# Kernel tuning notes

Hardware: AMD Instinct MI355X
Metric: run time of the kernel (lower is better)

The kernel has to match this reference:

```python
import jax, jax.numpy as jnp
import numpy as np
from jax import lax

B, T, D, H, W = 2, 8, 64, 64, 64
E, HID = 4, 256


def _layernorm(x, g, b, eps=1e-5):
    m = x.mean(-1, keepdims=True)
    v = ((x - m) ** 2).mean(-1, keepdims=True)
    return (x - m) / jnp.sqrt(v + eps) * g + b


def _pscan(A, X, axis):
    # linear recurrence h_t = A_t * h_{t-1} + X_t via associative scan
    def comb(l, r):
        a1, x1 = l
        a2, x2 = r
        return a2 * a1, a2 * x1 + x2
    return lax.associative_scan(comb, (A, X), axis=axis)[1]


def setup_inputs() -> dict:
    key = jax.random.key(0)
    ks = jax.random.split(key, 32)
    r = lambda i, shape, s=1.0: jax.random.normal(ks[i], shape, jnp.float32) * s
    D2 = 2 * D
    return {
        'x_re': r(0, (B, T, D, H, W)), 'x_im': r(1, (B, T, D, H, W)),
        'dt': jax.random.uniform(ks[2], (T,), jnp.float32, 0.5, 1.0),
        'ln_s_g': jnp.ones(D2), 'ln_s_b': jnp.zeros(D2),
        'conv_w': r(3, (3, 3, D2, D2), 0.03), 'conv_b': jnp.zeros(D2),
        'mom_w': r(4, (D2, D2), 0.08), 'mom_b': jnp.zeros(D2),
        'adv_w': jnp.full((1,), 0.1, jnp.float32),
        'enc_re': r(5, (D, D), 0.1), 'enc_im': r(6, (D, D), 0.1),
        'dec_re': r(7, (D, D), 0.1), 'dec_im': r(8, (D, D), 0.1),
        'flux_a_re': r(9, (D,)), 'flux_a_im': r(10, (D,), 0.1),
        'fin_re': r(11, (D, D), 0.1), 'fin_im': r(12, (D, D), 0.1),
        'fproj_re': r(13, (D, D), 0.1), 'fproj_im': r(14, (D, D), 0.1),
        'gate_w': r(15, (D2, D), 0.1), 'gate_b': jnp.zeros(D),
        'lam_re': r(16, (D,)), 'lam_im': r(17, (D,), 0.1),
        'noise_re': r(18, (B, T, H, W, D)), 'noise_im': r(19, (B, T, H, W, D)),
        'e_scale': jnp.full((1,), 0.1, jnp.float32),
        'ln_t_g': jnp.ones(D2), 'ln_t_b': jnp.zeros(D2),
        'router_w': r(20, (D2, E), 0.1), 'router_b': jnp.zeros(E),
        'w1': r(21, (E, D2, HID), 0.08), 'b1': jnp.zeros((E, HID)),
        'w2': r(22, (E, HID, D2), 0.08), 'b2': jnp.zeros((E, D2)),
    }


def _forward(x_re, x_im, dt, ln_s_g, ln_s_b, conv_w, conv_b, mom_w, mom_b, adv_w,
             enc_re, enc_im, dec_re, dec_im, flux_a_re, flux_a_im, fin_re, fin_im,
             fproj_re, fproj_im, gate_w, gate_b, lam_re, lam_im, noise_re, noise_im,
             e_scale, ln_t_g, ln_t_b, router_w, router_b, w1, b1, w2, b2):
    x = (x_re + 1j * x_im).astype(jnp.complex64)            # [B,T,D,H,W]
    target_energy = (jnp.abs(x) ** 2).mean(axis=(-2, -1))   # [B,T,D]
    momentum = x.mean(axis=(-2, -1))                        # [B,T,D] complex
    xcl = jnp.transpose(x, (0, 1, 3, 4, 2))                 # [B,T,H,W,D]
    Bs, Ts, Hs, Ws, Ds = xcl.shape
    D2 = 2 * Ds
    # --- spatial complex (Clifford) conv branch: LN over 2D channels + conv ---
    xr = jnp.concatenate([xcl.real, xcl.imag], -1)          # [B,T,H,W,2D]
    xn = _layernorm(xr, ln_s_g, ln_s_b)
    y = lax.conv_general_dilated(xn.reshape(Bs * Ts, Hs, Ws, D2), conv_w,
                                 (1, 1), 'SAME',
                                 dimension_numbers=('NHWC', 'HWIO', 'NHWC')) + conv_b
    y = y.reshape(Bs, Ts, Hs, Ws, D2)
    xcl = xcl + (y[..., :Ds] + 1j * y[..., Ds:])
    # --- momentum advection ---
    z_mean = xcl.mean(axis=(2, 3))                          # [B,T,D]
    mom_cat = jnp.concatenate([momentum.real, momentum.imag], -1) @ mom_w + mom_b
    mom_new = mom_cat[..., :Ds] + 1j * mom_cat[..., Ds:]
    dtb = jnp.broadcast_to(dt[None, :], (Bs, Ts))
    xcl = xcl + (mom_new * adv_w[0])[:, :, None, None, :] * dtb[:, :, None, None, None]
    momentum = 0.9 * momentum + 0.1 * z_mean
    # --- eigenbasis encode ---
    x_eigen = xcl @ (enc_re + 1j * enc_im)                  # [B,T,H,W,D]
    x_mean = x_eigen.mean(axis=(2, 3))                      # [B,T,D]
    # --- flux tracker: parallel scan over T ---
    A_flux = jnp.exp(-jax.nn.softplus(flux_a_re) + 1j * flux_a_im)
    A_flux = jnp.broadcast_to(A_flux, (Bs, Ts, Ds)).astype(jnp.complex64)
    X_flux = x_mean @ (fin_re + 1j * fin_im)
    flux_seq = _pscan(A_flux, X_flux, axis=1)               # [B,T,D]
    source = flux_seq @ (fproj_re + 1j * fproj_im)
    gate = jax.nn.sigmoid(jnp.concatenate([flux_seq.real, flux_seq.imag], -1) @ gate_w + gate_b)
    g = gate[:, :, None, None, :]
    forcing = x_eigen * g + source[:, :, None, None, :] * (1.0 - g)
    # --- temporal propagation: per-site parallel scan over T ---
    lam = -jax.nn.softplus(lam_re) + 1j * lam_im            # [D]
    op_decay = jnp.exp(lam[None, None, :] * dtb[:, :, None])  # [B,T,D]
    op_forcing = (op_decay - 1.0) / lam
    u_t = forcing * op_forcing[:, :, None, None, :]
    A_time = jnp.broadcast_to(op_decay[:, :, None, None, :], u_t.shape)
    u_out = _pscan(A_time, u_t, axis=1)                     # [B,T,H,W,D]
    noise = 0.01 * jnp.sqrt(dtb)[:, :, None, None, None] * (noise_re + 1j * noise_im)
    u_out = u_out + noise
    # --- decode + energy projection ---
    x_out = u_out @ (dec_re + 1j * dec_im)                  # [B,T,H,W,D]
    cur_e = (jnp.abs(x_out) ** 2).mean(axis=(2, 3))
    ratio = jnp.clip(target_energy / (cur_e + 1e-8), 0.5, 2.0)
    sf = jnp.sqrt(ratio)[:, :, None, None, :]
    x_out = x_out * (1.0 + e_scale[0] * (sf - 1.0))
    # --- temporal LN + MoE FFN on real-concat tokens ---
    xr2 = jnp.concatenate([x_out.real, x_out.imag], -1)
    xn2 = _layernorm(xr2, ln_t_g, ln_t_b)                   # [B,T,H,W,2D]
    tok = xn2.reshape(-1, D2)                               # [N,2D]
    p = jax.nn.softmax(tok @ router_w + router_b, -1)       # [N,E]
    hmid = jax.nn.gelu(jnp.einsum('nd,edh->neh', tok, w1) + b1)
    eout = jnp.einsum('neh,ehd->ned', hmid, w2) + b2
    out_tok = tok + jnp.einsum('ne,ned->nd', p, eout)
    out = out_tok.reshape(Bs, Ts, Hs, Ws, D2)
    x_out_c = out[..., :Ds] + 1j * out[..., Ds:]
    z_out = xcl + x_out_c
    z = jnp.transpose(z_out, (0, 1, 4, 2, 3))               # [B,T,D,H,W]
    return jnp.stack([z.real, z.imag])                      # [2,B,T,D,H,W]


def reference(x_re, x_im, dt, ln_s_g, ln_s_b, conv_w, conv_b, mom_w, mom_b, adv_w,
              enc_re, enc_im, dec_re, dec_im, flux_a_re, flux_a_im, fin_re, fin_im,
              fproj_re, fproj_im, gate_w, gate_b, lam_re, lam_im, noise_re, noise_im,
              e_scale, ln_t_g, ln_t_b, router_w, router_b, w1, b1, w2, b2):
    return _forward(x_re, x_im, dt, ln_s_g, ln_s_b, conv_w, conv_b, mom_w, mom_b, adv_w,
                    enc_re, enc_im, dec_re, dec_im, flux_a_re, flux_a_im, fin_re, fin_im,
                    fproj_re, fproj_im, gate_w, gate_b, lam_re, lam_im, noise_re, noise_im,
                    e_scale, ln_t_g, ln_t_b, router_w, router_b, w1, b1, w2, b2)
```

## Files before the change

### kernel.cpp

```cpp
#include <hip/hip_runtime.h>
#include <hip/hip_bf16.h>
#include <math.h>


#define W_XB     4194304u
#define W_C      8388608u
#define W_CWT    12582912u
#define W_W1T    14680064u
#define W_W2T    14745600u
#define W_ENCM   14811136u
#define W_DECM   14819328u
#define W_XMP_RE 14827520u
#define W_XMP_IM 14893056u
#define W_EP_RE  14958592u
#define W_EP_IM  15220736u
#define W_XMR    15482880u
#define W_XMI    15483904u
#define W_FLR    15484928u
#define W_FLI    15485952u
#define W_EIG_RE 16777216u
#define W_K1R    20971520u
#define W_K1I    21037056u
#define W_K1E    21102592u
#define W_SMALL  25165824u
#define W_TE     (W_SMALL+0u)
#define W_MTRE   (W_SMALL+3072u)
#define W_MTIM   (W_SMALL+4096u)
#define W_GATE   (W_SMALL+5120u)
#define W_SRCRE  (W_SMALL+6144u)
#define W_SRCIM  (W_SMALL+7168u)
#define W_OPFRE  (W_SMALL+8192u)
#define W_OPFIM  (W_SMALL+9216u)
#define W_OPDRE  (W_SMALL+10240u)
#define W_OPDIM  (W_SMALL+11264u)
#define W_SCALE  (W_SMALL+12288u)

#define XB_IM 4194304u

typedef __attribute__((ext_vector_type(8))) short bf16x8;
typedef __attribute__((ext_vector_type(4))) float f32x4;

__device__ __forceinline__ unsigned short bfr(float x) {
  __hip_bfloat16 h = __float2bfloat16(x);
  return *(unsigned short*)&h;
}
__device__ __forceinline__ unsigned int pk2(float a, float b) {
  return ((unsigned int)bfr(b) << 16) | (unsigned int)bfr(a);
}
__device__ __forceinline__ float sb2f(short s) {
  return __uint_as_float(((unsigned int)(unsigned short)s) << 16);
}
__device__ __forceinline__ float softplusf(float x) {
  return (x > 20.f) ? x : log1pf(expf(x));
}

__global__ __launch_bounds__(256) void k2_transpose_ln(
    const float* __restrict__ xre, const float* __restrict__ xim,
    const float* __restrict__ g, const float* __restrict__ bb_, float* ws) {
  int blk = blockIdx.x; int bt = blk >> 6, h = blk & 63;
  __shared__ float tre[64][65], tim[64][65];
  __shared__ float mean_l[64], rstd_l[64];
  int tid = threadIdx.x;
  size_t inbase = (size_t)bt * 262144 + (size_t)h * 64;
  for (int i = tid; i < 1024; i += 256) {
    int d = i >> 4, w4 = (i & 15) * 4;
    float4 vr = *(const float4*)&xre[inbase + (size_t)d * 4096 + w4];
    float4 vi = *(const float4*)&xim[inbase + (size_t)d * 4096 + w4];
    tre[d][w4] = vr.x; tre[d][w4 + 1] = vr.y; tre[d][w4 + 2] = vr.z; tre[d][w4 + 3] = vr.w;
    tim[d][w4] = vi.x; tim[d][w4 + 1] = vi.y; tim[d][w4 + 2] = vi.z; tim[d][w4 + 3] = vi.w;
  }
  __syncthreads();
  {
    int w = tid >> 2, part = tid & 3;
    float s = 0.f, sq = 0.f;
    for (int dd = part * 16; dd < part * 16 + 16; dd++) {
      float vr = tre[dd][w], vi = tim[dd][w];
      s += vr + vi; sq += vr * vr + vi * vi;
    }
    s += __shfl_xor(s, 1);  s += __shfl_xor(s, 2);
    sq += __shfl_xor(sq, 1); sq += __shfl_xor(sq, 2);
    if (part == 0) {
      float m = s / 128.f, v = sq / 128.f - m * m;
      mean_l[w] = m; rstd_l[w] = rsqrtf(v + 1e-5f);
    }
  }
  {
    int d = tid >> 2, part = tid & 3;
    float sr = 0.f, si = 0.f, se = 0.f;
    for (int w2 = part * 16; w2 < part * 16 + 16; w2++) {
      float vr = tre[d][w2], vi = tim[d][w2];
      sr += vr; si += vi; se += vr * vr + vi * vi;
    }
    sr += __shfl_xor(sr, 1); sr += __shfl_xor(sr, 2);
    si += __shfl_xor(si, 1); si += __shfl_xor(si, 2);
    se += __shfl_xor(se, 1); se += __shfl_xor(se, 2);
    if (part == 0) {
      int idx = h * 1024 + bt * 64 + d;
      ws[W_K1R + idx] = sr; ws[W_K1I + idx] = si; ws[W_K1E + idx] = se;
    }
  }
  {
    __hip_bfloat16* xbb = (__hip_bfloat16*)(ws + W_XB);
    for (int i = tid; i < 1024; i += 256) {
      int d = i >> 4, w4 = (i & 15) * 4;
      size_t ob = (size_t)(bt * 64 + d) * 4096 + (size_t)h * 64 + w4;
      *(unsigned int*)&xbb[ob]     = pk2(tre[d][w4],     tre[d][w4 + 1]);
      *(unsigned int*)&xbb[ob + 2] = pk2(tre[d][w4 + 2], tre[d][w4 + 3]);
      *(unsigned int*)&xbb[XB_IM + ob]     = pk2(tim[d][w4],     tim[d][w4 + 1]);
      *(unsigned int*)&xbb[XB_IM + ob + 2] = pk2(tim[d][w4 + 2], tim[d][w4 + 3]);
    }
  }
  __syncthreads();
  size_t tokbase = (size_t)blk * 64;
  __hip_bfloat16* xnb = (__hip_bfloat16*)(ws + W_C);
  int c0 = (tid & 63) * 2, wg = tid >> 6;
  float gc0 = g[c0], bc0 = bb_[c0], gc1 = g[c0 + 1], bc1 = bb_[c0 + 1];
  for (int pass = 0; pass < 16; pass++) {
    int w = pass * 4 + wg;
    float m = mean_l[w], rs = rstd_l[w];
    float v0 = (c0 < 64) ? tre[c0][w] : tim[c0 - 64][w];
    float v1 = (c0 + 1 < 64) ? tre[c0 + 1][w] : tim[c0 + 1 - 64][w];
    *(unsigned int*)&xnb[tokbase * 128 + (size_t)w * 128 + c0] =
        pk2((v0 - m) * rs * gc0 + bc0, (v1 - m) * rs * gc1 + bc1);
  }
}

__global__ void k1b2b(const float* __restrict__ mom_w, const float* __restrict__ mom_b,
                      const float* __restrict__ adv_w, const float* __restrict__ dt, float* ws) {
  int bt = blockIdx.x; int t = bt & 7;
  __shared__ float mc[128], outl[128];
  int tid = threadIdx.x;
  if (tid < 64) {
    int d = tid;
    float a = 0.f, b = 0.f, c = 0.f;
    for (int h = 0; h < 64; h++) {
      int idx = h * 1024 + bt * 64 + d;
      a += ws[W_K1R + idx]; b += ws[W_K1I + idx]; c += ws[W_K1E + idx];
    }
    ws[W_TE + bt * 64 + d] = c / 4096.f;
    mc[d] = a / 4096.f;
    mc[64 + d] = b / 4096.f;
  }
  __syncthreads();
  float acc = mom_b[tid];
  for (int k = 0; k < 128; k++) acc += mc[k] * mom_w[k * 128 + tid];
  outl[tid] = acc;
  __syncthreads();
  if (tid < 64) {
    float f = adv_w[0] * dt[t];
    ws[W_MTRE + bt * 64 + tid] = outl[tid] * f;
    ws[W_MTIM + bt * 64 + tid] = outl[64 + tid] * f;
  }
}

__global__ void k0_wprep(const float* __restrict__ w1, const float* __restrict__ w2,
                         const float* __restrict__ cw,
                         const float* __restrict__ enc_re, const float* __restrict__ enc_im,
                         const float* __restrict__ dec_re, const float* __restrict__ dec_im,
                         float* ws) {
  __hip_bfloat16* w1f = (__hip_bfloat16*)(ws + W_W1T);
  __hip_bfloat16* w2f = (__hip_bfloat16*)(ws + W_W2T);
  __hip_bfloat16* cwt = (__hip_bfloat16*)(ws + W_CWT);
  __hip_bfloat16* encM = (__hip_bfloat16*)(ws + W_ENCM);
  __hip_bfloat16* decM = (__hip_bfloat16*)(ws + W_DECM);
  int idx = blockIdx.x * 256 + threadIdx.x;
  if (idx < 131072) {
    {
      int j = idx & 7, lane = (idx >> 3) & 63, kt = (idx >> 9) & 3, nt = (idx >> 11) & 15, e = idx >> 15;
      int cout = nt * 16 + (lane & 15);
      int cin = kt * 32 + (lane >> 4) * 8 + j;
      w1f[idx] = __float2bfloat16(w1[((size_t)(e * 128 + cin)) * 256 + cout]);
    }
    {
      int j = idx & 7, lane = (idx >> 3) & 63, kt = (idx >> 9) & 7, nt = (idx >> 12) & 7, e = idx >> 15;
      int cout = nt * 16 + (lane & 15);
      int cin = kt * 32 + (lane >> 4) * 8 + j;
      w2f[idx] = __float2bfloat16(w2[((size_t)(e * 256 + cin)) * 128 + cout]);
    }
  }
  if (idx < 147456) {
    int j = idx & 7, lane = (idx >> 3) & 63, kt = (idx >> 9) & 3, r = idx >> 11;
    int nt = r & 7, tap = r >> 3;
    int cout = nt * 16 + (lane & 15);
    int cin = kt * 32 + (lane >> 4) * 8 + j;
    cwt[idx] = __float2bfloat16(cw[((size_t)(tap * 128 + cin)) * 128 + cout]);
  }
  if (idx < 16384) {
    int jj = idx & 7, lane = (idx >> 3) & 63, kt = (idx >> 9) & 3, nt = idx >> 11;
    int jc = nt * 16 + (lane & 15);
    int k = kt * 32 + (lane >> 4) * 8 + jj;
    float ve, vd;
    if (k < 64) {
      ve = (jc < 64) ? enc_re[k * 64 + jc] : enc_im[k * 64 + (jc - 64)];
      vd = (jc < 64) ? dec_re[k * 64 + jc] : dec_im[k * 64 + (jc - 64)];
    } else {
      int kk = k - 64;
      ve = (jc < 64) ? -enc_im[kk * 64 + jc] : enc_re[kk * 64 + (jc - 64)];
      vd = (jc < 64) ? -dec_im[kk * 64 + jc] : dec_re[kk * 64 + (jc - 64)];
    }
    encM[idx] = __float2bfloat16(ve);
    decM[idx] = __float2bfloat16(vd);
  }
}

__global__ __launch_bounds__(256) void k3_conv_enc(const float* __restrict__ cb, float* ws) {
  int blk = blockIdx.x; int bt = blk >> 6, h = blk & 63;
  const __hip_bfloat16* xnb = (const __hip_bfloat16*)(ws + W_C);
  const __hip_bfloat16* cwt = (const __hip_bfloat16*)(ws + W_CWT);
  const __hip_bfloat16* encM = (const __hip_bfloat16*)(ws + W_ENCM);
  const __hip_bfloat16* xbb = (const __hip_bfloat16*)(ws + W_XB);
  __hip_bfloat16* xclb = (__hip_bfloat16*)ws;
  __hip_bfloat16* eigb = (__hip_bfloat16*)(ws + W_EIG_RE);
  __shared__ __align__(16) char smem[3 * 66 * 136 * 2];
  __hip_bfloat16 (*xin)[66][136] = (__hip_bfloat16(*)[66][136])smem;
  char* A = smem;
  int tid = threadIdx.x, lane = tid & 63, wv = tid >> 6;
  int arow = lane & 15, kgrp = (lane >> 4) * 8, rbase = (lane >> 4) * 4;

  for (int r = 0; r < 3; r++) {
    int hh = h + r - 1;
    if (hh < 0 || hh >= 64) {
      unsigned int* z = (unsigned int*)&xin[r][0][0];
      for (int i = tid; i < 4488; i += 256) z[i] = 0u;
    } else {
      if (tid < 68) *(unsigned int*)&xin[r][0][tid * 2] = 0u;
      else if (tid < 136) *(unsigned int*)&xin[r][65][(tid - 136 + 68) * 2] = 0u;
      const __hip_bfloat16* src = xnb + ((size_t)bt * 4096 + (size_t)hh * 64) * 128;
      for (int i = tid; i < 1024; i += 256) {
        int wp = (i >> 4) + 1, c8 = (i & 15) * 8;
        *(bf16x8*)&xin[r][wp][c8] = *(const bf16x8*)&src[(size_t)(wp - 1) * 128 + c8];
      }
    }
  }
  __syncthreads();

  f32x4 oacc[4][2];
  #pragma unroll
  for (int m = 0; m < 4; m++) {
    oacc[m][0] = (f32x4){0.f, 0.f, 0.f, 0.f};
    oacc[m][1] = (f32x4){0.f, 0.f, 0.f, 0.f};
  }

  for (int tap = 0; tap < 9; tap++) {
    int kh = tap / 3, kw = tap % 3;
    const __hip_bfloat16* wt0 = cwt + ((size_t)(tap * 8 + wv * 2) * 4) * 512 + lane * 8;
    #pragma unroll
    for (int kt = 0; kt < 4; kt++) {
      bf16x8 a[4];
      #pragma unroll
      for (int m = 0; m < 4; m++)
        a[m] = *(const bf16x8*)&xin[kh][m * 16 + arow + kw][kt * 32 + kgrp];
      bf16x8 b0 = *(const bf16x8*)&wt0[(size_t)kt * 512];
      bf16x8 b1 = *(const bf16x8*)&wt0[(size_t)(kt + 4) * 512];
      #pragma unroll
      for (int m = 0; m < 4; m++) {
        oacc[m][0] = __builtin_amdgcn_mfma_f32_16x16x32_bf16(a[m], b0, oacc[m][0], 0, 0, 0);
        oacc[m][1] = __builtin_amdgcn_mfma_f32_16x16x32_bf16(a[m], b1, oacc[m][1], 0, 0, 0);
      }
    }
  }
  __syncthreads();

  size_t rowtok = (size_t)blk * 64;
  #pragma unroll
  for (int n = 0; n < 2; n++) {
    int cout = (wv * 2 + n) * 16 + arow;
    bool isre = cout < 64;
    int d = cout & 63;
    float add = cb[cout] + ws[(isre ? W_MTRE : W_MTIM) + bt * 64 + d];
    size_t xb = isre ? 0u : XB_IM;
    const __hip_bfloat16* xsrc = xbb + xb + (size_t)(bt * 64 + d) * 4096 + (size_t)h * 64;
    #pragma unroll
    for (int m = 0; m < 4; m++) {
      unsigned int u0 = *(const unsigned int*)&xsrc[m * 16 + rbase];
      unsigned int u1 = *(const unsigned int*)&xsrc[m * 16 + rbase + 2];
      float xo0 = __uint_as_float(u0 << 16);
      float xo1 = __uint_as_float(u0 & 0xffff0000u);
      float xo2 = __uint_as_float(u1 << 16);
      float xo3 = __uint_as_float(u1 & 0xffff0000u);
      #pragma unroll
      for (int r = 0; r < 4; r++) {
        int w = m * 16 + rbase + r;
        float xo = (r == 0) ? xo0 : (r == 1) ? xo1 : (r == 2) ? xo2 : xo3;
        float v = xo + oacc[m][n][r] + add;
        xclb[xb + (rowtok + w) * 64 + d] = __float2bfloat16(v);
        *(__hip_bfloat16*)(A + w * 256 + ((cout * 2) ^ ((w & 7) << 4))) = __float2bfloat16(v);
      }
    }
  }
  __syncthreads();

  f32x4 acc[4][2];
  #pragma unroll
  for (int m = 0; m < 4; m++) {
    acc[m][0] = (f32x4){0.f, 0.f, 0.f, 0.f};
    acc[m][1] = (f32x4){0.f, 0.f, 0.f, 0.f};
  }
  #pragma unroll
  for (int kt = 0; kt < 4; kt++) {
    bf16x8 a[4];
    #pragma unroll
    for (int m = 0; m < 4; m++)
      a[m] = *(const bf16x8*)(A + (m * 16 + arow) * 256 + (((kt * 32 + kgrp) * 2) ^ ((arow & 7) << 4)));
    bf16x8 b0 = *(const bf16x8*)&encM[(((size_t)(wv * 2 + 0) * 4 + kt) * 64 + lane) * 8];
    bf16x8 b1 = *(const bf16x8*)&encM[(((size_t)(wv * 2 + 1) * 4 + kt) * 64 + lane) * 8];
    #pragma unroll
    for (int m = 0; m < 4; m++) {
      acc[m][0] = __builtin_amdgcn_mfma_f32_16x16x32_bf16(a[m], b0, acc[m][0], 0, 0, 0);
      acc[m][1] = __builtin_amdgcn_mfma_f32_16x16x32_bf16(a[m], b1, acc[m][1], 0, 0, 0);
    }
  }
  #pragma unroll
  for (int n = 0; n < 2; n++) {
    int jc = (wv * 2 + n) * 16 + arow;
    size_t eb = (jc < 64) ? 0u : XB_IM;
    int col = jc & 63;
    #pragma unroll
    for (int m = 0; m < 4; m++)
      #pragma unroll
      for (int r = 0; r < 4; r++)
        eigb[eb + (rowtok + m * 16 + rbase + r) * 64 + col] = __float2bfloat16(acc[m][n][r]);
    float s = 0.f;
    #pragma unroll
    for (int m = 0; m < 4; m++)
      #pragma unroll
      for (int r = 0; r < 4; r++) s += acc[m][n][r];
    s += __shfl_xor(s, 16);
    s += __shfl_xor(s, 32);
    if (lane < 16)
      ws[(jc < 64 ? W_XMP_RE : W_XMP_IM) + (size_t)blk * 64 + col] = s;
  }
}

__global__ void k6a_xm(float* ws) {
  int bt = blockIdx.x, j = threadIdx.x;
  float sr = 0.f, si = 0.f;
  for (int q = 0; q < 64; q++) {
    sr += ws[W_XMP_RE + (size_t)(bt * 64 + q) * 64 + j];
    si += ws[W_XMP_IM + (size_t)(bt * 64 + q) * 64 + j];
  }
  ws[W_XMR + bt * 64 + j] = sr / 4096.f;
  ws[W_XMI + bt * 64 + j] = si / 4096.f;
}

__global__ void k6b_flux(const float* __restrict__ fin_re, const float* __restrict__ fin_im,
                         const float* __restrict__ flux_a_re, const float* __restrict__ flux_a_im,
                         float* ws) {
  __shared__ float Xfr[1024], Xfi[1024];
  int tid = threadIdx.x;
  for (int i = tid; i < 1024; i += 256) {
    int bt = i >> 6, j = i & 63;
    float ar = 0.f, ai = 0.f;
    for (int d = 0; d < 64; d++) {
      float xr = ws[W_XMR + bt * 64 + d], xi = ws[W_XMI + bt * 64 + d];
      float wr = fin_re[d * 64 + j], wi = fin_im[d * 64 + j];
      ar += xr * wr - xi * wi; ai += xr * wi + xi * wr;
    }
    Xfr[i] = ar; Xfi[i] = ai;
  }
  __syncthreads();
  if (tid < 128) {
    int b = tid >> 6, j = tid & 63;
    float mag = expf(-softplusf(flux_a_re[j]));
    float aar = mag * cosf(flux_a_im[j]), aai = mag * sinf(flux_a_im[j]);
    float sr = 0.f, si = 0.f;
    for (int t = 0; t < 8; t++) {
      int idx = (b * 8 + t) * 64 + j;
      float nr = aar * sr - aai * si + Xfr[idx];
      float ni = aar * si + aai * sr + Xfi[idx];
      sr = nr; si = ni;
      ws[W_FLR + idx] = sr; ws[W_FLI + idx] = si;
    }
  }
}

__global__ void k6c_gate(const float* __restrict__ fproj_re, const float* __restrict__ fproj_im,
                         const float* __restrict__ gate_w, const float* __restrict__ gate_b,
                         const float* __restrict__ lam_re, const float* __restrict__ lam_im,
                         const float* __restrict__ dt, float* ws) {
  int bt = blockIdx.x;
  __shared__ float flr[64], fli[64];
  int tid = threadIdx.x;
  if (tid < 64) { flr[tid] = ws[W_FLR + bt * 64 + tid]; fli[tid] = ws[W_FLI + bt * 64 + tid]; }
  __syncthreads();
  int j = tid >> 2, part = tid & 3;
  float ar = 0.f, ai = 0.f, lg = 0.f;
  for (int d = part * 16; d < part * 16 + 16; d++) {
    float fr = flr[d], fi = fli[d];
    float wr = fproj_re[d * 64 + j], wi = fproj_im[d * 64 + j];
    ar += fr * wr - fi * wi; ai += fr * wi + fi * wr;
    lg += fr * gate_w[d * 64 + j] + fi * gate_w[(64 + d) * 64 + j];
  }
  ar += __shfl_xor(ar, 1); ar += __shfl_xor(ar, 2);
  ai += __shfl_xor(ai, 1); ai += __shfl_xor(ai, 2);
  lg += __shfl_xor(lg, 1); lg += __shfl_xor(lg, 2);
  if (part == 0) {
    int idx = bt * 64 + j;
    ws[W_SRCRE + idx] = ar; ws[W_SRCIM + idx] = ai;
    ws[W_GATE + idx] = 1.f / (1.f + expf(-(lg + gate_b[j])));
  }
  if (tid < 64) {
    int d = tid, t = bt & 7;
    float lr = -softplusf(lam_re[d]), li = lam_im[d];
    float dtv = dt[t];
    float mag = expf(lr * dtv);
    float dr = mag * cosf(li * dtv), di = mag * sinf(li * dtv);
    int idx = bt * 64 + d;
    ws[W_OPDRE + idx] = dr; ws[W_OPDIM + idx] = di;
    float omr = dr - 1.f, omi = di;
    float den = lr * lr + li * li;
    ws[W_OPFRE + idx] = (omr * lr + omi * li) / den;
    ws[W_OPFIM + idx] = (omi * lr - omr * li) / den;
  }
}

__global__ __launch_bounds__(256) void k7_dec(const float* __restrict__ nre,
                                              const float* __restrict__ nim,
                                              const float* __restrict__ dt, float* ws) {
  int blk = blockIdx.x;
  int b = blk >> 8, h = (blk >> 2) & 63, wq = blk & 3;
  const __hip_bfloat16* decM = (const __hip_bfloat16*)(ws + W_DECM);
  __hip_bfloat16* eigb = (__hip_bfloat16*)(ws + W_EIG_RE);
  __shared__ float gl[8][64], srl[8][64], sil[8][64], ofr[8][64], ofi[8][64], odr[8][64], odi[8][64];
  __shared__ __align__(16) char A[2][4096];
  __shared__ float dts[8];
  int tid = threadIdx.x, lane = tid & 63, wv = tid >> 6;
  int arow = lane & 15, kgrp = (lane >> 4) * 8, rbase = (lane >> 4) * 4;
  for (int i = tid; i < 512; i += 256) {
    int t = i >> 6, d = i & 63, idx = (b * 8 + t) * 64 + d;
    gl[t][d]  = ws[W_GATE + idx];
    srl[t][d] = ws[W_SRCRE + idx]; sil[t][d] = ws[W_SRCIM + idx];
    ofr[t][d] = ws[W_OPFRE + idx]; ofi[t][d] = ws[W_OPFIM + idx];
    odr[t][d] = ws[W_OPDRE + idx]; odi[t][d] = ws[W_OPDIM + idx];
  }
  if (tid < 8) dts[tid] = dt[tid];
  __syncthreads();

  int dp = (tid & 31) * 2, wslot = tid >> 5;
  float ur[2][2], ui[2][2];
  #pragma unroll
  for (int a_ = 0; a_ < 2; a_++) { ur[a_][0] = 0.f; ur[a_][1] = 0.f; ui[a_][0] = 0.f; ui[a_][1] = 0.f; }

  for (int t = 0; t < 8; t++) {
    float ns = 0.01f * sqrtf(dts[t]);
    size_t tokb = ((size_t)(b * 8 + t) * 64 + h) * 64 + (size_t)wq * 16;
    char* At = A[t & 1];
    float g0 = gl[t][dp],  g1 = gl[t][dp + 1];
    float s0 = srl[t][dp], s1 = srl[t][dp + 1];
    float q0 = sil[t][dp], q1 = sil[t][dp + 1];
    float f0 = ofr[t][dp], f1 = ofr[t][dp + 1];
    float e0 = ofi[t][dp], e1 = ofi[t][dp + 1];
    float r0 = odr[t][dp], r1 = odr[t][dp + 1];
    float o0 = odi[t][dp], o1 = odi[t][dp + 1];
    #pragma unroll
    for (int wi = 0; wi < 2; wi++) {
      int wl = wslot + wi * 8;
      size_t off = (tokb + wl) * 64 + dp;
      unsigned int re2 = *(const unsigned int*)&eigb[off];
      unsigned int im2 = *(const unsigned int*)&eigb[XB_IM + off];
      float2 nr2 = *(const float2*)&nre[off];
      float2 ni2 = *(const float2*)&nim[off];
      float uo0, vo0, uo1, vo1;
      {
        float er_ = __uint_as_float(re2 << 16);
        float ei_ = __uint_as_float(im2 << 16);
        float fre = er_ * g0 + s0 * (1.f - g0);
        float fim = ei_ * g0 + q0 * (1.f - g0);
        float utr = fre * f0 - fim * e0;
        float uti = fre * e0 + fim * f0;
        float nur = r0 * ur[wi][0] - o0 * ui[wi][0] + utr;
        float nui = r0 * ui[wi][0] + o0 * ur[wi][0] + uti;
        ur[wi][0] = nur; ui[wi][0] = nui;
        uo0 = nur + ns * nr2.x; vo0 = nui + ns * ni2.x;
      }
      {
        float er_ = __uint_as_float(re2 & 0xffff0000u);
        float ei_ = __uint_as_float(im2 & 0xffff0000u);
        float fre = er_ * g1 + s1 * (1.f - g1);
        float fim = ei_ * g1 + q1 * (1.f - g1);
        float utr = fre * f1 - fim * e1;
        float uti = fre * e1 + fim * f1;
        float nur = r1 * ur[wi][1] - o1 * ui[wi][1] + utr;
        float nui = r1 * ui[wi][1] + o1 * ur[wi][1] + uti;
        ur[wi][1] = nur; ui[wi][1] = nui;
        uo1 = nur + ns * nr2.y; vo1 = nui + ns * ni2.y;
      }
      int sw = (wl & 7) << 4;
      *(unsigned int*)(At + wl * 256 + ((dp * 2) ^ sw)) = pk2(uo0, uo1);
      *(unsigned int*)(At + wl * 256 + ((128 + dp * 2) ^ sw)) = pk2(vo0, vo1);
    }
    __syncthreads();
    f32x4 acc[2];
    acc[0] = (f32x4){0.f, 0.f, 0.f, 0.f};
    acc[1] = (f32x4){0.f, 0.f, 0.f, 0.f};
    #pragma unroll
    for (int kt = 0; kt < 4; kt++) {
      bf16x8 a0 = *(const bf16x8*)(At + arow * 256 + (((kt * 32 + kgrp) * 2) ^ ((arow & 7) << 4)));
      bf16x8 b0 = *(const bf16x8*)&decM[(((size_t)(wv * 2 + 0) * 4 + kt) * 64 + lane) * 8];
      bf16x8 b1 = *(const bf16x8*)&decM[(((size_t)(wv * 2 + 1) * 4 + kt) * 64 + lane) * 8];
      acc[0] = __builtin_amdgcn_mfma_f32_16x16x32_bf16(a0, b0, acc[0], 0, 0, 0);
      acc[1] = __builtin_amdgcn_mfma_f32_16x16x32_bf16(a0, b1, acc[1], 0, 0, 0);
    }
    #pragma unroll
    for (int n = 0; n < 2; n++) {
      int jc = (wv * 2 + n) * 16 + arow;
      size_t eb = (jc < 64) ? 0u : XB_IM;
      int col = jc & 63;
      #pragma unroll
      for (int r = 0; r < 4; r++)
        eigb[eb + (tokb + rbase + r) * 64 + col] = __float2bfloat16(acc[n][r]);
      float s = acc[n][0] * acc[n][0] + acc[n][1] * acc[n][1]
              + acc[n][2] * acc[n][2] + acc[n][3] * acc[n][3];
      s += __shfl_xor(s, 16);
      s += __shfl_xor(s, 32);
      if (lane < 16)
        ws[(jc < 64 ? W_EP_RE : W_EP_IM)
           + (size_t)((b * 8 + t) * 256 + h * 4 + wq) * 64 + col] = s;
    }
  }
}

__global__ void k9b_scale(const float* __restrict__ escale, float* ws) {
  int bt = blockIdx.x; int j = threadIdx.x;
  float s = 0.f;
  for (int q = 0; q < 256; q++) {
    size_t idx = (size_t)(bt * 256 + q) * 64 + j;
    s += ws[W_EP_RE + idx] + ws[W_EP_IM + idx];
  }
  float cur = s / 4096.f;
  float te = ws[W_TE + bt * 64 + j];
  float ratio = te / (cur + 1e-8f);
  ratio = fminf(fmaxf(ratio, 0.5f), 2.0f);
  ws[W_SCALE + bt * 64 + j] = 1.f + escale[0] * (sqrtf(ratio) - 1.f);
}

__global__ __launch_bounds__(512) void k11_moe(
    const float* __restrict__ rw, const float* __restrict__ rb,
    const float* __restrict__ b1, const float* __restrict__ b2,
    const float* __restrict__ g2, const float* __restrict__ b2_,
    float* __restrict__ ws, float* __restrict__ out) {
  int blk = blockIdx.x; int bt = blk >> 6, h = blk & 63;
  const __hip_bfloat16* w1f = (const __hip_bfloat16*)(ws + W_W1T);
  const __hip_bfloat16* w2f = (const __hip_bfloat16*)(ws + W_W2T);
  const __hip_bfloat16* xclb = (const __hip_bfloat16*)ws;
  const __hip_bfloat16* eigb = (const __hip_bfloat16*)(ws + W_EIG_RE);
  __shared__ __align__(16) char smem[147456];
  __shared__ float pl[64][4];
  char* lt = smem;
  int tid = threadIdx.x, lane = tid & 63, wv = tid >> 6;
  int arow = lane & 15, kgrp = (lane >> 4) * 8, rbase = (lane >> 4) * 4;
  size_t tokbase = (size_t)blk * 64;

  int w = tid >> 3, part = tid & 7;
  int c0 = part * 16, dbase = (part & 3) * 16;
  const __hip_bfloat16* rp = eigb + ((part < 4) ? 0u : XB_IM) + (tokbase + w) * 64 + dbase;
  const float* scg = ws + W_SCALE + bt * 64 + dbase;
  float an[16];
  {
    bf16x8 h0 = *(const bf16x8*)rp;
    bf16x8 h1 = *(const bf16x8*)(rp + 8);
    float f[16];
    #pragma unroll
    for (int j = 0; j < 8; j++) {
      f[j]     = sb2f(h0[j]) * scg[j];
      f[8 + j] = sb2f(h1[j]) * scg[8 + j];
    }
    float s = 0.f, sq = 0.f;
    #pragma unroll
    for (int k = 0; k < 16; k++) { s += f[k]; sq += f[k] * f[k]; }
    s  += __shfl_xor(s, 1);  s  += __shfl_xor(s, 2);  s  += __shfl_xor(s, 4);
    sq += __shfl_xor(sq, 1); sq += __shfl_xor(sq, 2); sq += __shfl_xor(sq, 4);
    float m = s / 128.f, v = sq / 128.f - m * m;
    float rstd = rsqrtf(v + 1e-5f);
    int szw = (w & 7) << 4;
    #pragma unroll
    for (int q = 0; q < 4; q++) {
      int c = c0 + q * 4;
      float a0 = (f[q * 4 + 0] - m) * rstd * g2[c]     + b2_[c];
      float a1 = (f[q * 4 + 1] - m) * rstd * g2[c + 1] + b2_[c + 1];
      float a2 = (f[q * 4 + 2] - m) * rstd * g2[c + 2] + b2_[c + 2];
      float a3 = (f[q * 4 + 3] - m) * rstd * g2[c + 3] + b2_[c + 3];
      an[q * 4 + 0] = a0; an[q * 4 + 1] = a1; an[q * 4 + 2] = a2; an[q * 4 + 3] = a3;
      *(unsigned int*)(lt + w * 256 + ((c * 2) ^ szw)) = pk2(a0, a1);
      *(unsigned int*)(lt + w * 256 + (((c + 2) * 2) ^ szw)) = pk2(a2, a3);
    }
    float l0 = 0.f, l1 = 0.f, l2 = 0.f, l3 = 0.f;
    #pragma unroll
    for (int k = 0; k < 16; k++) {
      float4 r4 = *(const float4*)&rw[(c0 + k) * 4];
      l0 += an[k] * r4.x; l1 += an[k] * r4.y; l2 += an[k] * r4.z; l3 += an[k] * r4.w;
    }
    l0 += __shfl_xor(l0, 1); l0 += __shfl_xor(l0, 2); l0 += __shfl_xor(l0, 4);
    l1 += __shfl_xor(l1, 1); l1 += __shfl_xor(l1, 2); l1 += __shfl_xor(l1, 4);
    l2 += __shfl_xor(l2, 1); l2 += __shfl_xor(l2, 2); l2 += __shfl_xor(l2, 4);
    l3 += __shfl_xor(l3, 1); l3 += __shfl_xor(l3, 2); l3 += __shfl_xor(l3, 4);
    l0 += rb[0]; l1 += rb[1]; l2 += rb[2]; l3 += rb[3];
    float mx = fmaxf(fmaxf(l0, l1), fmaxf(l2, l3));
    float e0 = expf(l0 - mx), e1 = expf(l1 - mx), e2 = expf(l2 - mx), e3 = expf(l3 - mx);
    float rs = __builtin_amdgcn_rcpf(e0 + e1 + e2 + e3);
    if (part == 0) {
      float4 p; p.x = e0 * rs; p.y = e1 * rs; p.z = e2 * rs; p.w = e3 * rs;
      *(float4*)&pl[w][0] = p;
    }
  }
  __syncthreads();

  f32x4 oacc[4];
  #pragma unroll
  for (int m = 0; m < 4; m++) {
    int col = wv * 16 + arow;
    oacc[m] = (f32x4){0.f, 0.f, 0.f, 0.f};
    #pragma unroll
    for (int r = 0; r < 4; r++) {
      int row = m * 16 + rbase + r;
      oacc[m][r] = __bfloat162float(
          *(const __hip_bfloat16*)(lt + row * 256 + ((col * 2) ^ ((row & 7) << 4))));
    }
  }

  for (int e = 0; e < 4; e++) {
    char* hb = smem + 16384 + e * 32768;
    f32x4 acc1[4][2];
    #pragma unroll
    for (int m = 0; m < 4; m++) {
      acc1[m][0] = (f32x4){0.f, 0.f, 0.f, 0.f};
      acc1[m][1] = (f32x4){0.f, 0.f, 0.f, 0.f};
    }
    #pragma unroll
    for (int kt = 0; kt < 4; kt++) {
      bf16x8 a[4];
      #pragma unroll
      for (int m = 0; m < 4; m++) {
        int row = m * 16 + arow;
        a[m] = *(const bf16x8*)(lt + row * 256 + (((kt * 32 + kgrp) * 2) ^ ((arow & 7) << 4)));
      }
      bf16x8 b0 = *(const bf16x8*)&w1f[(((size_t)(e * 16 + wv * 2 + 0) * 4 + kt) * 64 + lane) * 8];
      bf16x8 b1 = *(const bf16x8*)&w1f[(((size_t)(e * 16 + wv * 2 + 1) * 4 + kt) * 64 + lane) * 8];
      #pragma unroll
      for (int m = 0; m < 4; m++) {
        acc1[m][0] = __builtin_amdgcn_mfma_f32_16x16x32_bf16(a[m], b0, acc1[m][0], 0, 0, 0);
        acc1[m][1] = __builtin_amdgcn_mfma_f32_16x16x32_bf16(a[m], b1, acc1[m][1], 0, 0, 0);
      }
    }
    #pragma unroll
    for (int n = 0; n < 2; n++) {
      int col = (wv * 2 + n) * 16 + arow;
      float bv = b1[e * 256 + col];
      #pragma unroll
      for (int m = 0; m < 4; m++)
        #pragma unroll
        for (int r = 0; r < 4; r++) {
          float hv = acc1[m][n][r] + bv;
          float z = 1.5957691216f * hv + 0.0713548162f * hv * hv * hv;
          float gelu = hv * __builtin_amdgcn_rcpf(1.f + __expf(-z));
          int row = m * 16 + rbase + r;
          *(__hip_bfloat16*)(hb + row * 512 + ((col * 2) ^ ((row & 7) << 4))) =
              __float2bfloat16(gelu);
        }
    }
  }
  __syncthreads();

  for (int e = 0; e < 4; e++) {
    const char* hb = smem + 16384 + e * 32768;
    f32x4 acc2[4];
    #pragma unroll
    for (int m = 0; m < 4; m++) acc2[m] = (f32x4){0.f, 0.f, 0.f, 0.f};
    #pragma unroll
    for (int kt = 0; kt < 8; kt++) {
      bf16x8 a2[4];
      #pragma unroll
      for (int m = 0; m < 4; m++) {
        int row = m * 16 + arow;
        a2[m] = *(const bf16x8*)(hb + row * 512 + (((kt * 32 + kgrp) * 2) ^ ((arow & 7) << 4)));
      }
      bf16x8 bb = *(const bf16x8*)&w2f[(((size_t)(e * 8 + wv) * 8 + kt) * 64 + lane) * 8];
      #pragma unroll
      for (int m = 0; m < 4; m++)
        acc2[m] = __builtin_amdgcn_mfma_f32_16x16x32_bf16(a2[m], bb, acc2[m], 0, 0, 0);
    }
    {
      int col = wv * 16 + arow;
      float bv2 = b2[e * 128 + col];
      #pragma unroll
      for (int m = 0; m < 4; m++)
        #pragma unroll
        for (int r = 0; r < 4; r++)
          oacc[m][r] += pl[m * 16 + rbase + r][e] * (acc2[m][r] + bv2);
    }
  }

  {
    int col = wv * 16 + arow;
    size_t xb = (col < 64) ? 0u : XB_IM;
    int dd = col & 63;
    size_t obase = (size_t)(col >> 6) * 4194304 + (size_t)bt * 262144
                 + (size_t)dd * 4096 + (size_t)h * 64;
    #pragma unroll
    for (int m = 0; m < 4; m++) {
      int wtb = m * 16 + rbase;
      float4 v;
      #pragma unroll
      for (int r = 0; r < 4; r++) {
        float res = __bfloat162float(xclb[xb + (tokbase + wtb + r) * 64 + dd]);
        ((float*)&v)[r] = oacc[m][r] + res;
      }
      *(float4*)&out[obase + wtb] = v;
    }
  }
}

extern "C" void kernel_launch(void* const* d_in, const int* in_sizes, int n_in,
                              void* d_out, int out_size, void* d_ws, size_t ws_size,
                              hipStream_t stream) {
  const float* x_re      = (const float*)d_in[0];
  const float* x_im      = (const float*)d_in[1];
  const float* dt        = (const float*)d_in[2];
  const float* ln_s_g    = (const float*)d_in[3];
  const float* ln_s_b    = (const float*)d_in[4];
  const float* conv_w    = (const float*)d_in[5];
  const float* conv_b    = (const float*)d_in[6];
  const float* mom_w     = (const float*)d_in[7];
  const float* mom_b     = (const float*)d_in[8];
  const float* adv_w     = (const float*)d_in[9];
  const float* enc_re    = (const float*)d_in[10];
  const float* enc_im    = (const float*)d_in[11];
  const float* dec_re    = (const float*)d_in[12];
  const float* dec_im    = (const float*)d_in[13];
  const float* flux_a_re = (const float*)d_in[14];
  const float* flux_a_im = (const float*)d_in[15];
  const float* fin_re    = (const float*)d_in[16];
  const float* fin_im    = (const float*)d_in[17];
  const float* fproj_re  = (const float*)d_in[18];
  const float* fproj_im  = (const float*)d_in[19];
  const float* gate_w    = (const float*)d_in[20];
  const float* gate_b    = (const float*)d_in[21];
  const float* lam_re    = (const float*)d_in[22];
  const float* lam_im    = (const float*)d_in[23];
  const float* noise_re  = (const float*)d_in[24];
  const float* noise_im  = (const float*)d_in[25];
  const float* e_scale   = (const float*)d_in[26];
  const float* ln_t_g    = (const float*)d_in[27];
  const float* ln_t_b    = (const float*)d_in[28];
  const float* router_w  = (const float*)d_in[29];
  const float* router_b  = (const float*)d_in[30];
  const float* w1        = (const float*)d_in[31];
  const float* b1        = (const float*)d_in[32];
  const float* w2        = (const float*)d_in[33];
  const float* b2        = (const float*)d_in[34];
  float* ws  = (float*)d_ws;
  float* out = (float*)d_out;

  k0_wprep<<<576, 256, 0, stream>>>(w1, w2, conv_w, enc_re, enc_im, dec_re, dec_im, ws);
  k2_transpose_ln<<<1024, 256, 0, stream>>>(x_re, x_im, ln_s_g, ln_s_b, ws);
  k1b2b<<<16, 128, 0, stream>>>(mom_w, mom_b, adv_w, dt, ws);
  k3_conv_enc<<<1024, 256, 0, stream>>>(conv_b, ws);
  k6a_xm<<<16, 64, 0, stream>>>(ws);
  k6b_flux<<<1, 256, 0, stream>>>(fin_re, fin_im, flux_a_re, flux_a_im, ws);
  k6c_gate<<<16, 256, 0, stream>>>(fproj_re, fproj_im, gate_w, gate_b, lam_re, lam_im, dt, ws);
  k7_dec<<<512, 256, 0, stream>>>(noise_re, noise_im, dt, ws);
  k9b_scale<<<16, 64, 0, stream>>>(e_scale, ws);
  k11_moe<<<1024, 512, 0, stream>>>(router_w, router_b, b1, b2, ln_t_g, ln_t_b, ws, out);
}
```

Measured before the change: 227.0 us.

## Halve MoE tile to 32 tokens, double-buffer hidden per expert, swap MFMA operands

The MoE kernel now handles 32 tokens per block with 256 threads over 2048 blocks, where it used to handle 64 tokens with 512 threads. Shared memory drops from about 144KB to 40KB because the per-expert GELU hidden buffer is ping-ponged across experts instead of all four being held at once. The first GEMM swaps operands so weights are the A fragment, which lets the GELU output be packed and stored as 64-bit writes. This aims to raise occupancy and shrink the LDS footprint. In exchange it adds a barrier per expert and reloads the expert weights twice as often in total.

```diff
diff --git a/kernel.cpp b/kernel.cpp
--- a/kernel.cpp
+++ b/kernel.cpp
@@ -53,6 +53,10 @@
 __device__ __forceinline__ float softplusf(float x) {
   return (x > 20.f) ? x : log1pf(expf(x));
 }
+__device__ __forceinline__ float gelu_f(float hv) {
+  float z = 1.5957691216f * hv + 0.0713548162f * hv * hv * hv;
+  return hv * __builtin_amdgcn_rcpf(1.f + __expf(-z));
+}
 
 __global__ __launch_bounds__(256) void k2_transpose_ln(
     const float* __restrict__ xre, const float* __restrict__ xim,
@@ -534,22 +538,24 @@
   ws[W_SCALE + bt * 64 + j] = 1.f + escale[0] * (sqrtf(ratio) - 1.f);
 }
 
-__global__ __launch_bounds__(512) void k11_moe(
+__global__ __launch_bounds__(256) void k11_moe(
     const float* __restrict__ rw, const float* __restrict__ rb,
     const float* __restrict__ b1, const float* __restrict__ b2,
     const float* __restrict__ g2, const float* __restrict__ b2_,
     float* __restrict__ ws, float* __restrict__ out) {
-  int blk = blockIdx.x; int bt = blk >> 6, h = blk & 63;
+  int blk = blockIdx.x;
+  int bt = blk >> 7, rest = blk & 127;
+  int h = rest >> 1, half = rest & 1;
   const __hip_bfloat16* w1f = (const __hip_bfloat16*)(ws + W_W1T);
   const __hip_bfloat16* w2f = (const __hip_bfloat16*)(ws + W_W2T);
   const __hip_bfloat16* xclb = (const __hip_bfloat16*)ws;
   const __hip_bfloat16* eigb = (const __hip_bfloat16*)(ws + W_EIG_RE);
-  __shared__ __align__(16) char smem[147456];
-  __shared__ float pl[64][4];
+  __shared__ __align__(16) char smem[40960];
+  __shared__ float pl[32][4];
   char* lt = smem;
   int tid = threadIdx.x, lane = tid & 63, wv = tid >> 6;
   int arow = lane & 15, kgrp = (lane >> 4) * 8, rbase = (lane >> 4) * 4;
-  size_t tokbase = (size_t)blk * 64;
+  size_t tokbase = (size_t)blk * 32;
 
   int w = tid >> 3, part = tid & 7;
   int c0 = part * 16, dbase = (part & 3) * 16;
@@ -605,105 +611,111 @@
   }
   __syncthreads();
 
-  f32x4 oacc[4];
+  f32x4 oacc[2][2];
   #pragma unroll
-  for (int m = 0; m < 4; m++) {
-    int col = wv * 16 + arow;
-    oacc[m] = (f32x4){0.f, 0.f, 0.f, 0.f};
-    #pragma unroll
-    for (int r = 0; r < 4; r++) {
-      int row = m * 16 + rbase + r;
-      oacc[m][r] = __bfloat162float(
-          *(const __hip_bfloat16*)(lt + row * 256 + ((col * 2) ^ ((row & 7) << 4))));
-    }
-  }
+  for (int m = 0; m < 2; m++)
+    #pragma unroll
+    for (int n = 0; n < 2; n++) {
+      int col = wv * 32 + n * 16 + arow;
+      oacc[m][n] = (f32x4){0.f, 0.f, 0.f, 0.f};
+      #pragma unroll
+      for (int r = 0; r < 4; r++) {
+        int row = m * 16 + rbase + r;
+        oacc[m][n][r] = __bfloat162float(
+            *(const __hip_bfloat16*)(lt + row * 256 + ((col * 2) ^ ((row & 7) << 4))));
+      }
+    }
 
   for (int e = 0; e < 4; e++) {
-    char* hb = smem + 16384 + e * 32768;
+    char* hb = smem + 8192 + (e & 1) * 16384;
     f32x4 acc1[4][2];
     #pragma unroll
-    for (int m = 0; m < 4; m++) {
-      acc1[m][0] = (f32x4){0.f, 0.f, 0.f, 0.f};
-      acc1[m][1] = (f32x4){0.f, 0.f, 0.f, 0.f};
+    for (int ht = 0; ht < 4; ht++) {
+      acc1[ht][0] = (f32x4){0.f, 0.f, 0.f, 0.f};
+      acc1[ht][1] = (f32x4){0.f, 0.f, 0.f, 0.f};
     }
     #pragma unroll
     for (int kt = 0; kt < 4; kt++) {
-      bf16x8 a[4];
-      #pragma unroll
-      for (int m = 0; m < 4; m++) {
-        int row = m * 16 + arow;
-        a[m] = *(const bf16x8*)(lt + row * 256 + (((kt * 32 + kgrp) * 2) ^ ((arow & 7) << 4)));
-      }
-      bf16x8 b0 = *(const bf16x8*)&w1f[(((size_t)(e * 16 + wv * 2 + 0) * 4 + kt) * 64 + lane) * 8];
-      bf16x8 b1 = *(const bf16x8*)&w1f[(((size_t)(e * 16 + wv * 2 + 1) * 4 + kt) * 64 + lane) * 8];
-      #pragma unroll
-      for (int m = 0; m < 4; m++) {
-        acc1[m][0] = __builtin_amdgcn_mfma_f32_16x16x32_bf16(a[m], b0, acc1[m][0], 0, 0, 0);
-        acc1[m][1] = __builtin_amdgcn_mfma_f32_16x16x32_bf16(a[m], b1, acc1[m][1], 0, 0, 0);
-      }
-    }
-    #pragma unroll
-    for (int n = 0; n < 2; n++) {
-      int col = (wv * 2 + n) * 16 + arow;
-      float bv = b1[e * 256 + col];
-      #pragma unroll
-      for (int m = 0; m < 4; m++)
-        #pragma unroll
-        for (int r = 0; r < 4; r++) {
-          float hv = acc1[m][n][r] + bv;
-          float z = 1.5957691216f * hv + 0.0713548162f * hv * hv * hv;
-          float gelu = hv * __builtin_amdgcn_rcpf(1.f + __expf(-z));
-          int row = m * 16 + rbase + r;
-          *(__hip_bfloat16*)(hb + row * 512 + ((col * 2) ^ ((row & 7) << 4))) =
-              __float2bfloat16(gelu);
-        }
-    }
-  }
-  __syncthreads();
-
-  for (int e = 0; e < 4; e++) {
-    const char* hb = smem + 16384 + e * 32768;
-    f32x4 acc2[4];
-    #pragma unroll
-    for (int m = 0; m < 4; m++) acc2[m] = (f32x4){0.f, 0.f, 0.f, 0.f};
+      bf16x8 bfrag[2];
+      #pragma unroll
+      for (int tt = 0; tt < 2; tt++) {
+        int row = tt * 16 + arow;
+        bfrag[tt] = *(const bf16x8*)(lt + row * 256 + (((kt * 32 + kgrp) * 2) ^ ((arow & 7) << 4)));
+      }
+      bf16x8 afrag[4];
+      #pragma unroll
+      for (int ht = 0; ht < 4; ht++)
+        afrag[ht] = *(const bf16x8*)&w1f[(((size_t)(e * 16 + wv * 4 + ht) * 4 + kt) * 64 + lane) * 8];
+      #pragma unroll
+      for (int ht = 0; ht < 4; ht++) {
+        acc1[ht][0] = __builtin_amdgcn_mfma_f32_16x16x32_bf16(afrag[ht], bfrag[0], acc1[ht][0], 0, 0, 0);
+        acc1[ht][1] = __builtin_amdgcn_mfma_f32_16x16x32_bf16(afrag[ht], bfrag[1], acc1[ht][1], 0, 0, 0);
+      }
+    }
+    #pragma unroll
+    for (int ht = 0; ht < 4; ht++) {
+      int hid0 = (wv * 4 + ht) * 16 + rbase;
+      float4 bv4 = *(const float4*)&b1[e * 256 + hid0];
+      #pragma unroll
+      for (int tt = 0; tt < 2; tt++) {
+        int token = tt * 16 + arow;
+        unsigned int lo = pk2(gelu_f(acc1[ht][tt][0] + bv4.x), gelu_f(acc1[ht][tt][1] + bv4.y));
+        unsigned int hi = pk2(gelu_f(acc1[ht][tt][2] + bv4.z), gelu_f(acc1[ht][tt][3] + bv4.w));
+        int bo = (hid0 * 2) ^ ((token & 7) << 4);
+        *(unsigned long long*)(hb + token * 512 + bo) =
+            ((unsigned long long)hi << 32) | (unsigned long long)lo;
+      }
+    }
+    __syncthreads();
+    f32x4 acc2[2][2];
+    #pragma unroll
+    for (int m = 0; m < 2; m++) {
+      acc2[m][0] = (f32x4){0.f, 0.f, 0.f, 0.f};
+      acc2[m][1] = (f32x4){0.f, 0.f, 0.f, 0.f};
+    }
     #pragma unroll
     for (int kt = 0; kt < 8; kt++) {
-      bf16x8 a2[4];
-      #pragma unroll
-      for (int m = 0; m < 4; m++) {
+      bf16x8 a2[2];
+      #pragma unroll
+      for (int m = 0; m < 2; m++) {
         int row = m * 16 + arow;
         a2[m] = *(const bf16x8*)(hb + row * 512 + (((kt * 32 + kgrp) * 2) ^ ((arow & 7) << 4)));
       }
-      bf16x8 bb = *(const bf16x8*)&w2f[(((size_t)(e * 8 + wv) * 8 + kt) * 64 + lane) * 8];
-      #pragma unroll
-      for (int m = 0; m < 4; m++)
-        acc2[m] = __builtin_amdgcn_mfma_f32_16x16x32_bf16(a2[m], bb, acc2[m], 0, 0, 0);
-    }
-    {
-      int col = wv * 16 + arow;
+      bf16x8 bb0 = *(const bf16x8*)&w2f[(((size_t)(e * 8 + wv * 2 + 0) * 8 + kt) * 64 + lane) * 8];
+      bf16x8 bb1 = *(const bf16x8*)&w2f[(((size_t)(e * 8 + wv * 2 + 1) * 8 + kt) * 64 + lane) * 8];
+      #pragma unroll
+      for (int m = 0; m < 2; m++) {
+        acc2[m][0] = __builtin_amdgcn_mfma_f32_16x16x32_bf16(a2[m], bb0, acc2[m][0], 0, 0, 0);
+        acc2[m][1] = __builtin_amdgcn_mfma_f32_16x16x32_bf16(a2[m], bb1, acc2[m][1], 0, 0, 0);
+      }
+    }
+    #pragma unroll
+    for (int n = 0; n < 2; n++) {
+      int col = wv * 32 + n * 16 + arow;
       float bv2 = b2[e * 128 + col];
       #pragma unroll
-      for (int m = 0; m < 4; m++)
+      for (int m = 0; m < 2; m++)
         #pragma unroll
         for (int r = 0; r < 4; r++)
-          oacc[m][r] += pl[m * 16 + rbase + r][e] * (acc2[m][r] + bv2);
-    }
-  }
-
-  {
-    int col = wv * 16 + arow;
+          oacc[m][n][r] += pl[m * 16 + rbase + r][e] * (acc2[m][n][r] + bv2);
+    }
+  }
+
+  #pragma unroll
+  for (int n = 0; n < 2; n++) {
+    int col = wv * 32 + n * 16 + arow;
     size_t xb = (col < 64) ? 0u : XB_IM;
     int dd = col & 63;
     size_t obase = (size_t)(col >> 6) * 4194304 + (size_t)bt * 262144
-                 + (size_t)dd * 4096 + (size_t)h * 64;
-    #pragma unroll
-    for (int m = 0; m < 4; m++) {
+                 + (size_t)dd * 4096 + (size_t)h * 64 + (size_t)half * 32;
+    #pragma unroll
+    for (int m = 0; m < 2; m++) {
       int wtb = m * 16 + rbase;
       float4 v;
       #pragma unroll
       for (int r = 0; r < 4; r++) {
         float res = __bfloat162float(xclb[xb + (tokbase + wtb + r) * 64 + dd]);
-        ((float*)&v)[r] = oacc[m][r] + res;
+        ((float*)&v)[r] = oacc[m][n][r] + res;
       }
       *(float4*)&out[obase + wtb] = v;
     }
@@ -760,5 +772,5 @@
   k6c_gate<<<16, 256, 0, stream>>>(fproj_re, fproj_im, gate_w, gate_b, lam_re, lam_im, dt, ws);
   k7_dec<<<512, 256, 0, stream>>>(noise_re, noise_im, dt, ws);
   k9b_scale<<<16, 64, 0, stream>>>(e_scale, ws);
-  k11_moe<<<1024, 512, 0, stream>>>(router_w, router_b, b1, b2, ln_t_g, ln_t_b, ws, out);
-}
+  k11_moe<<<2048, 256, 0, stream>>>(router_w, router_b, b1, b2, ln_t_g, ln_t_b, ws, out);
+}
```

New measurement: 231.7 us. +2.1%, slower.
